# Optimization experiments

Hardware: AMD Instinct MI355X
Metric: run time of the kernel (lower is better)

The kernel has to match this reference:

```python
import jax, jax.numpy as jnp
import numpy as np

B, T, D, SD, CHUNK = 4, 4096, 1024, 512, 32


def setup_inputs() -> dict:
    key = jax.random.key(0)
    ks = jax.random.split(key, 6)
    sc_in = 1.0 / np.sqrt(D)
    sc_out = 1.0 / np.sqrt(2 * SD)
    return {
        "x": jax.random.normal(ks[0], (B, T, D), jnp.float32),
        "Wt": jax.random.normal(ks[1], (D, SD), jnp.float32) * sc_in,
        "bt": jnp.zeros((SD,), jnp.float32),
        "Wr": jax.random.normal(ks[2], (D, SD), jnp.float32) * sc_in,
        "br": jnp.zeros((SD,), jnp.float32),
        "Wi": jax.random.normal(ks[3], (D, 2 * SD), jnp.float32) * sc_in,
        "bi": jnp.zeros((2 * SD,), jnp.float32),
        "Wo": jax.random.normal(ks[4], (2 * SD, D), jnp.float32) * sc_out,
        "bo": jnp.zeros((D,), jnp.float32),
        "gamma": jnp.ones((D,), jnp.float32),
        "beta": jnp.zeros((D,), jnp.float32),
    }


def _rotation_scan(theta, retain, b_r, b_i, chunk):
    # theta/retain/b_*: [B, T, d]. Chunked linear recurrence h[t]=a[t]*h[t-1]+b[t]
    # with a[t] = retain[t]*e^{i theta[t]}, done in log-magnitude/angle space.
    Bsz, Tlen, d = theta.shape
    K = min(chunk, Tlen)
    n = Tlen // K  # T assumed divisible by K (4096 / 32)
    resh = lambda a: a.reshape(Bsz, n, K, d).transpose(1, 0, 2, 3)  # [n,B,K,d]
    th_c, rt_c, br_c, bi_c = resh(theta), resh(retain), resh(b_r), resh(b_i)

    def step(carry, xs):
        h_r, h_i = carry  # [B, d]
        th, rt, cb_r, cb_i = xs  # [B, K, d]
        cum_log_mag = jnp.cumsum(jnp.log(jnp.clip(rt, 1e-6, None)), axis=1)
        cum_mag = jnp.exp(cum_log_mag)
        cum_th = jnp.cumsum(th, axis=1)
        cum_cos = jnp.cos(cum_th)
        cum_sin = jnp.sin(cum_th)
        cum_a_r = cum_mag * cum_cos
        cum_a_i = cum_mag * cum_sin
        inv_mag = 1.0 / jnp.clip(cum_mag, 1e-8, None)
        inv_r = inv_mag * cum_cos          # cos(-t) = cos(t)
        inv_i = -inv_mag * cum_sin         # sin(-t) = -sin(t)
        scaled_b_r = inv_r * cb_r - inv_i * cb_i
        scaled_b_i = inv_r * cb_i + inv_i * cb_r
        cum_b_r = jnp.cumsum(scaled_b_r, axis=1)
        cum_b_i = jnp.cumsum(scaled_b_i, axis=1)
        tot_r = h_r[:, None] + cum_b_r
        tot_i = h_i[:, None] + cum_b_i
        ch_r = cum_a_r * tot_r - cum_a_i * tot_i
        ch_i = cum_a_r * tot_i + cum_a_i * tot_r
        return (ch_r[:, -1], ch_i[:, -1]), (ch_r, ch_i)

    h0 = (jnp.zeros((Bsz, d), theta.dtype), jnp.zeros((Bsz, d), theta.dtype))
    _, (out_r, out_i) = jax.lax.scan(step, h0, (th_c, rt_c, br_c, bi_c))
    back = lambda a: a.transpose(1, 0, 2, 3).reshape(Bsz, Tlen, d)
    return back(out_r), back(out_i)


def reference(x, Wt, bt, Wr, br, Wi, bi, Wo, bo, gamma, beta):
    d = Wt.shape[1]
    theta = x @ Wt + bt                       # [B,T,d]
    retain = jax.nn.sigmoid(x @ Wr + br)      # [B,T,d]
    inp = x @ Wi + bi                          # [B,T,2d]
    inp_r, inp_i = inp[..., :d], inp[..., d:]
    drive = 1.0 - retain
    out_r, out_i = _rotation_scan(theta, retain, drive * inp_r, drive * inp_i, CHUNK)
    out = jnp.concatenate([out_r, out_i], axis=-1)  # [B,T,2d]
    y = x + out @ Wo + bo
    mu = jnp.mean(y, axis=-1, keepdims=True)
    var = jnp.var(y, axis=-1, keepdims=True)
    return (y - mu) / jnp.sqrt(var + 1e-5) * gamma + beta
```

## Files before the change

kernel.cpp:

```cpp
#include <hip/hip_runtime.h>
#include <cstdint>


typedef __bf16 bf16x8 __attribute__((ext_vector_type(8)));
typedef float  f32x4  __attribute__((ext_vector_type(4)));
typedef ushort u16x8  __attribute__((ext_vector_type(8)));

#define AS1 __attribute__((address_space(1)))
#define AS3 __attribute__((address_space(3)))

__device__ __forceinline__ void gload16(const void* g, void* l) {
  __builtin_amdgcn_global_load_lds((const AS1 void*)g, (AS3 void*)l, 16, 0, 0);
}

__device__ __forceinline__ ushort f2bf(float f) {
  union { float f; uint32_t u; } v; v.f = f;
  uint32_t u = v.u;
  uint32_t r = u + 0x7FFFu + ((u >> 16) & 1u);
  return (ushort)(r >> 16);
}
__device__ __forceinline__ float bf2f(ushort u) {
  union { uint32_t x; float f; } v; v.x = (uint32_t)u << 16; return v.f;
}

__global__ __launch_bounds__(256) void tconv(const float* __restrict__ src, int R, int C,
                                             ushort* __restrict__ dst, int row_off) {
  __shared__ float tile[32][33];
  int tx = threadIdx.x, ty = threadIdx.y;
  int rb = blockIdx.y * 32, cb = blockIdx.x * 32;
#pragma unroll
  for (int yy = 0; yy < 4; ++yy) {
    int r = rb + ty + yy * 8;
    tile[ty + yy * 8][tx] = src[(size_t)r * C + cb + tx];
  }
  __syncthreads();
#pragma unroll
  for (int yy = 0; yy < 4; ++yy) {
    int c = cb + ty + yy * 8;
    dst[(size_t)(row_off + c) * R + rb + tx] = f2bf(tile[tx][ty + yy * 8]);
  }
}

__global__ __launch_bounds__(256) void pack_bias(const float* __restrict__ bt,
                                                 const float* __restrict__ br,
                                                 const float* __restrict__ bi,
                                                 float* __restrict__ bcat) {
  int i = blockIdx.x * 256 + threadIdx.x;
  bcat[i] = (i < 512) ? bt[i] : (i < 1024 ? br[i - 512] : bi[i - 1024]);
}

__global__ __launch_bounds__(256) void xconv(const float4* __restrict__ src,
                                             ushort* __restrict__ dst, int n4) {
  int i = blockIdx.x * 256 + threadIdx.x;
  if (i < n4) {
    float4 v = src[i];
    ushort4 o;
    o.x = f2bf(v.x); o.y = f2bf(v.y); o.z = f2bf(v.z); o.w = f2bf(v.w);
    *(ushort4*)(dst + (size_t)i * 4) = o;
  }
}

template <int BM>
__global__ __launch_bounds__(512, 2) void gemm256(const ushort* __restrict__ A,
                                                  const ushort* __restrict__ Bt,
                                                  ushort* __restrict__ C,
                                                  const float* __restrict__ bias,
                                                  int M, int N, int K, int nbn) {
  constexpr int MI = BM / 32;
  constexpr int II = BM / 128;
  constexpr int STAGE_USH = 2 * (BM * 64 + 256 * 64);
  constexpr int CT_USH = BM * 256;
  constexpr int SM_USH = (STAGE_USH > CT_USH) ? STAGE_USH : CT_USH;
  __shared__ alignas(16) ushort smem[SM_USH];
  ushort* const As0 = smem;
  ushort* const Bs0 = smem + 2 * BM * 64;

  const int cpx = gridDim.x >> 3;
  const int wg = ((int)blockIdx.x & 7) * cpx + ((int)blockIdx.x >> 3);
  const int bm = wg / nbn, bn = wg % nbn;

  const int t = threadIdx.x;
  const int l = t & 63, w = t >> 6;
  const int wm = w >> 2, wn = w & 3;
  const int r = l & 15, kq = l >> 4;

  const size_t a0 = (size_t)bm * BM * K;
  const size_t b0 = (size_t)bn * 256 * K;

  const int srow = t >> 3;
  const int sslot = (t & 7) ^ (srow & 7);
  const ushort* gA = A + a0 + (size_t)srow * K + sslot * 8;
  const ushort* gB = Bt + b0 + (size_t)srow * K + sslot * 8;
  const int lboff = w * 1024 + l * 16;

  f32x4 acc[MI][4] = {};
  const int NKT = K >> 6;

#define STGA(buf, kt, u) \
  gload16(gA + (size_t)((u) * 64) * K + (size_t)(kt) * 64, \
          (char*)(As0 + (buf) * BM * 64) + (u) * 8192 + lboff)
#define STGB(buf, kt, u) \
  gload16(gB + (size_t)((u) * 64) * K + (size_t)(kt) * 64, \
          (char*)(Bs0 + (buf) * 256 * 64) + (u) * 8192 + lboff)

#define QUAD(ph)                                                               \
  do {                                                                         \
    _Pragma("unroll")                                                          \
    for (int ii = 0; ii < II; ++ii) {                                          \
      bf16x8 aF[2];                                                            \
      const int rowa = wm * (BM / 2) + ((ph) * II + ii) * 16 + r;              \
      _Pragma("unroll")                                                        \
      for (int ks = 0; ks < 2; ++ks) {                                         \
        const int j = (ks * 4 + kq) ^ (r & 7);                                 \
        aF[ks] = *(const bf16x8*)&pA[rowa * 64 + j * 8];                       \
      }                                                                        \
      __builtin_amdgcn_s_setprio(1);                                           \
      _Pragma("unroll")                                                        \
      for (int jn = 0; jn < 4; ++jn)                                           \
        _Pragma("unroll")                                                      \
        for (int ks = 0; ks < 2; ++ks)                                         \
          acc[(ph) * II + ii][jn] = __builtin_amdgcn_mfma_f32_16x16x32_bf16(   \
              aF[ks], bF[jn][ks], acc[(ph) * II + ii][jn], 0, 0, 0);           \
      __builtin_amdgcn_s_setprio(0);                                           \
    }                                                                          \
  } while (0)

  STGB(0, 0, 0); STGB(0, 0, 1); STGB(0, 0, 2); STGB(0, 0, 3);
  if constexpr (BM == 256) { STGA(0, 0, 0); STGA(0, 0, 2); STGA(0, 0, 1); STGA(0, 0, 3); }
  else                     { STGA(0, 0, 0); STGA(0, 0, 1); }

  for (int kt = 0; kt < NKT; ++kt) {
    const int cur = kt & 1, nxt = cur ^ 1;
    const bool hn = (kt + 1 < NKT);
    const ushort* pA = As0 + cur * BM * 64;
    const ushort* pB = Bs0 + cur * 256 * 64;
    if (hn) { STGB(nxt, kt + 1, 0); STGB(nxt, kt + 1, 1); }
    if constexpr (BM == 256) {
      if (hn) asm volatile("s_waitcnt vmcnt(4)" ::: "memory");
      else    asm volatile("s_waitcnt vmcnt(2)" ::: "memory");
    } else {
      if (hn) asm volatile("s_waitcnt vmcnt(2)" ::: "memory");
      else    asm volatile("s_waitcnt vmcnt(0)" ::: "memory");
    }
    __builtin_amdgcn_s_barrier();
    asm volatile("" ::: "memory");
    bf16x8 bF[4][2];
#pragma unroll
    for (int jn = 0; jn < 4; ++jn) {
      const int rowb = wn * 64 + jn * 16 + r;
#pragma unroll
      for (int ks = 0; ks < 2; ++ks) {
        const int j = (ks * 4 + kq) ^ (r & 7);
        bF[jn][ks] = *(const bf16x8*)&pB[rowb * 64 + j * 8];
      }
    }
    QUAD(0);
    if (hn) { STGB(nxt, kt + 1, 2); STGB(nxt, kt + 1, 3); }
    QUAD(1);
    if (hn) {
      if constexpr (BM == 256) { STGA(nxt, kt + 1, 0); STGA(nxt, kt + 1, 2); }
      else                     { STGA(nxt, kt + 1, 0); }
    }
    if constexpr (BM == 256) {
      if (hn) asm volatile("s_waitcnt vmcnt(6)" ::: "memory");
      else    asm volatile("s_waitcnt vmcnt(0)" ::: "memory");
    }
    __builtin_amdgcn_s_barrier();
    asm volatile("" ::: "memory");
    QUAD(2);
    if (hn) {
      if constexpr (BM == 256) { STGA(nxt, kt + 1, 1); STGA(nxt, kt + 1, 3); }
      else                     { STGA(nxt, kt + 1, 1); }
    }
    QUAD(3);
  }
#undef STGA
#undef STGB
#undef QUAD

  asm volatile("s_waitcnt lgkmcnt(0) vmcnt(0)" ::: "memory");
  __builtin_amdgcn_s_barrier();

  const int q4 = (l >> 4) * 4;
  float bvj[4];
#pragma unroll
  for (int jn = 0; jn < 4; ++jn) {
    const int col = wn * 64 + jn * 16 + r;
    bvj[jn] = bias ? bias[bn * 256 + col] : 0.f;
  }
#pragma unroll
  for (int i = 0; i < MI; ++i) {
#pragma unroll
    for (int jn = 0; jn < 4; ++jn) {
      const int col = wn * 64 + jn * 16 + r;
      const int chunk = col >> 3;
#pragma unroll
      for (int q = 0; q < 4; ++q) {
        const int rowl = wm * (BM / 2) + i * 16 + q4 + q;
        const int pch = chunk ^ (rowl & 7);
        smem[rowl * 256 + pch * 8 + (col & 7)] = f2bf(acc[i][jn][q] + bvj[jn]);
      }
    }
  }
  __builtin_amdgcn_s_barrier();

  const int rrow0 = t >> 5;
  const int rch = t & 31;
#pragma unroll
  for (int p = 0; p < BM / 16; ++p) {
    const int rowl = p * 16 + rrow0;
    const int pch = rch ^ (rowl & 7);
    u16x8 vv = *(const u16x8*)&smem[rowl * 256 + pch * 8];
    const size_t grow = (size_t)(bm * BM + rowl);
    *(u16x8*)&C[grow * N + bn * 256 + rch * 8] = vv;
  }
}

__global__ __launch_bounds__(256) void scan_k1(const ushort* __restrict__ lin,
                                               float4* __restrict__ agg) {
  int bd = blockIdx.x * 256 + threadIdx.x;
  int c  = blockIdx.y;
  int b  = bd >> 9, d = bd & 511;
  const ushort* base = lin + ((size_t)b * 4096 + (size_t)c * 32) * 2048;
  float cth = 0.f, cbr = 0.f, cbi = 0.f;
  float cm = 1.f, cs = 1.f, sn = 0.f;
#pragma unroll 4
  for (int t = 0; t < 32; ++t) {
    const ushort* row = base + (size_t)t * 2048;
    float th = bf2f(row[d]);
    float z  = bf2f(row[512 + d]);
    float ir = bf2f(row[1024 + d]);
    float ii = bf2f(row[1536 + d]);
    float rt = __fdividef(1.f, 1.f + __expf(-z));
    cm *= fmaxf(rt, 1e-6f);
    cth += th;
    float s_, c_;
    __sincosf(cth, &s_, &c_);
    float im = __fdividef(1.f, fmaxf(cm, 1e-8f));
    float invr = im * c_, invi = -im * s_;
    float drive = 1.f - rt;
    float br_ = drive * ir, bi_ = drive * ii;
    cbr += invr * br_ - invi * bi_;
    cbi += invr * bi_ + invi * br_;
    cs = c_; sn = s_;
  }
  agg[(size_t)c * 2048 + bd] = make_float4(cm * cs, cm * sn, cbr, cbi);
}

__global__ __launch_bounds__(256) void scan_k2(const float4* __restrict__ agg,
                                               float2* __restrict__ h0) {
  int bd = blockIdx.x * 256 + threadIdx.x;
  float hr = 0.f, hi = 0.f;
  for (int cg = 0; cg < 16; ++cg) {
    float4 a[8];
#pragma unroll
    for (int u = 0; u < 8; ++u) a[u] = agg[(size_t)(cg * 8 + u) * 2048 + bd];
#pragma unroll
    for (int u = 0; u < 8; ++u) {
      h0[(size_t)(cg * 8 + u) * 2048 + bd] = make_float2(hr, hi);
      float tr = hr + a[u].z, ti = hi + a[u].w;
      hr = a[u].x * tr - a[u].y * ti;
      hi = a[u].x * ti + a[u].y * tr;
    }
  }
}

__global__ __launch_bounds__(256) void scan_k3(const ushort* __restrict__ lin,
                                               const float2* __restrict__ h0,
                                               ushort* __restrict__ outb) {
  int bd = blockIdx.x * 256 + threadIdx.x;
  int c  = blockIdx.y;
  int b  = bd >> 9, d = bd & 511;
  const ushort* base = lin + ((size_t)b * 4096 + (size_t)c * 32) * 2048;
  float2 h = h0[(size_t)c * 2048 + bd];
  float cth = 0.f, cbr = 0.f, cbi = 0.f, cm = 1.f;
#pragma unroll 4
  for (int t = 0; t < 32; ++t) {
    const ushort* row = base + (size_t)t * 2048;
    float th = bf2f(row[d]);
    float z  = bf2f(row[512 + d]);
    float ir = bf2f(row[1024 + d]);
    float ii = bf2f(row[1536 + d]);
    float rt = __fdividef(1.f, 1.f + __expf(-z));
    cm *= fmaxf(rt, 1e-6f);
    cth += th;
    float s_, c_;
    __sincosf(cth, &s_, &c_);
    float im = __fdividef(1.f, fmaxf(cm, 1e-8f));
    float invr = im * c_, invi = -im * s_;
    float drive = 1.f - rt;
    float br_ = drive * ir, bi_ = drive * ii;
    cbr += invr * br_ - invi * bi_;
    cbi += invr * bi_ + invi * br_;
    float ar = cm * c_, ai = cm * s_;
    float tr = h.x + cbr, ti = h.y + cbi;
    float orr = ar * tr - ai * ti;
    float oii = ar * ti + ai * tr;
    size_t rowo = ((size_t)b * 4096 + (size_t)c * 32 + t) * 1024;
    outb[rowo + d] = f2bf(orr);
    outb[rowo + 512 + d] = f2bf(oii);
  }
}

__global__ __launch_bounds__(256) void ln_k(const ushort* __restrict__ yb,
                                            const ushort* __restrict__ xb,
                                            const float* __restrict__ gamma,
                                            const float* __restrict__ beta,
                                            float* __restrict__ out) {
  int row = blockIdx.x;
  ushort4 uy = ((const ushort4*)(yb + (size_t)row * 1024))[threadIdx.x];
  ushort4 ux = ((const ushort4*)(xb + (size_t)row * 1024))[threadIdx.x];
  float4 v;
  v.x = bf2f(uy.x) + bf2f(ux.x);
  v.y = bf2f(uy.y) + bf2f(ux.y);
  v.z = bf2f(uy.z) + bf2f(ux.z);
  v.w = bf2f(uy.w) + bf2f(ux.w);
  float s  = v.x + v.y + v.z + v.w;
  float s2 = v.x * v.x + v.y * v.y + v.z * v.z + v.w * v.w;
#pragma unroll
  for (int off = 32; off > 0; off >>= 1) {
    s  += __shfl_down(s, off);
    s2 += __shfl_down(s2, off);
  }
  __shared__ float red[8];
  __shared__ float mv[2];
  int l = threadIdx.x & 63, w = threadIdx.x >> 6;
  if (l == 0) { red[w] = s; red[4 + w] = s2; }
  __syncthreads();
  if (threadIdx.x == 0) {
    float ts = red[0] + red[1] + red[2] + red[3];
    float t2 = red[4] + red[5] + red[6] + red[7];
    float mu = ts * (1.f / 1024.f);
    float var = t2 * (1.f / 1024.f) - mu * mu;
    mv[0] = mu;
    mv[1] = 1.f / sqrtf(var + 1e-5f);
  }
  __syncthreads();
  float mu = mv[0], rstd = mv[1];
  const float4* g4 = (const float4*)gamma;
  const float4* b4 = (const float4*)beta;
  float4 gv = g4[threadIdx.x], bv = b4[threadIdx.x];
  float4 o;
  o.x = (v.x - mu) * rstd * gv.x + bv.x;
  o.y = (v.y - mu) * rstd * gv.y + bv.y;
  o.z = (v.z - mu) * rstd * gv.z + bv.z;
  o.w = (v.w - mu) * rstd * gv.w + bv.w;
  ((float4*)(out + (size_t)row * 1024))[threadIdx.x] = o;
}

extern "C" void kernel_launch(void* const* d_in, const int* in_sizes, int n_in,
                              void* d_out, int out_size, void* d_ws, size_t ws_size,
                              hipStream_t stream) {
  (void)in_sizes; (void)n_in; (void)out_size; (void)ws_size;
  const float* x  = (const float*)d_in[0];
  const float* Wt = (const float*)d_in[1];
  const float* bt = (const float*)d_in[2];
  const float* Wr = (const float*)d_in[3];
  const float* br = (const float*)d_in[4];
  const float* Wi = (const float*)d_in[5];
  const float* bi = (const float*)d_in[6];
  const float* Wo = (const float*)d_in[7];
  const float* bo = (const float*)d_in[8];
  const float* gamma = (const float*)d_in[9];
  const float* beta  = (const float*)d_in[10];

  char* ws = (char*)d_ws;
  ushort* wcat_t = (ushort*)(ws);
  ushort* wo_t   = (ushort*)(ws + ((size_t)4  << 20));
  float*  bcat   = (float*) (ws + ((size_t)6  << 20));
  float4* agg    = (float4*)(ws + ((size_t)8  << 20));
  float2* h0     = (float2*)(ws + ((size_t)12 << 20));
  ushort* xb     = (ushort*)(ws + ((size_t)16 << 20));
  ushort* outb   = (ushort*)(ws + ((size_t)48 << 20));
  ushort* linb   = (ushort*)(ws + ((size_t)80 << 20));
  ushort* yb     = (ushort*)(ws + ((size_t)80 << 20));

  tconv<<<dim3(512 / 32, 1024 / 32), dim3(32, 8), 0, stream>>>(Wt, 1024, 512, wcat_t, 0);
  tconv<<<dim3(512 / 32, 1024 / 32), dim3(32, 8), 0, stream>>>(Wr, 1024, 512, wcat_t, 512);
  tconv<<<dim3(1024 / 32, 1024 / 32), dim3(32, 8), 0, stream>>>(Wi, 1024, 1024, wcat_t, 1024);
  tconv<<<dim3(1024 / 32, 1024 / 32), dim3(32, 8), 0, stream>>>(Wo, 1024, 1024, wo_t, 0);
  pack_bias<<<8, 256, 0, stream>>>(bt, br, bi, bcat);
  xconv<<<16384, 256, 0, stream>>>((const float4*)x, xb, 4194304);

  gemm256<256><<<512, 512, 0, stream>>>(xb, wcat_t, linb, bcat, 16384, 2048, 1024, 8);

  scan_k1<<<dim3(8, 128), 256, 0, stream>>>(linb, agg);
  scan_k2<<<8, 256, 0, stream>>>(agg, h0);
  scan_k3<<<dim3(8, 128), 256, 0, stream>>>(linb, h0, outb);

  gemm256<256><<<256, 512, 0, stream>>>(outb, wo_t, yb, bo, 16384, 1024, 1024, 4);

  ln_k<<<16384, 256, 0, stream>>>(yb, xb, gamma, beta, (float*)d_out);
}
```

Measured before the change: 210.6 us.

## Merge weight-transpose launches, reorder GEMM A-stage loads, use warp-per-row layernorm

The four weight transpose/convert launches become one 3D-grid kernel. In the GEMM main loop, the A fragments for the third quarter are read into registers before the next-stage A loads are issued, which drops one vmcnt wait and keeps MFMAs running across the barrier. The layernorm now gives each wavefront a full row and reduces with xor shuffles, removing shared-memory reductions and both __syncthreads. Together these aim to cut launch overhead and sync stalls, at the cost of a more fragile hand-written load/wait ordering in the GEMM.

```diff
diff --git a/kernel.cpp b/kernel.cpp
--- a/kernel.cpp
+++ b/kernel.cpp
@@ -23,8 +23,19 @@
   union { uint32_t x; float f; } v; v.x = (uint32_t)u << 16; return v.f;
 }
 
-__global__ __launch_bounds__(256) void tconv(const float* __restrict__ src, int R, int C,
-                                             ushort* __restrict__ dst, int row_off) {
+__global__ __launch_bounds__(256) void tconv_all(const float* __restrict__ Wt,
+                                                 const float* __restrict__ Wr,
+                                                 const float* __restrict__ Wi,
+                                                 const float* __restrict__ Wo,
+                                                 ushort* __restrict__ wcat,
+                                                 ushort* __restrict__ wot) {
+  const int z = blockIdx.z;
+  if (z < 2 && blockIdx.x >= 16) return;
+  const float* src = (z == 0) ? Wt : (z == 1) ? Wr : (z == 2) ? Wi : Wo;
+  const int C = (z < 2) ? 512 : 1024;
+  const int row_off = (z == 0) ? 0 : (z == 1) ? 512 : (z == 2) ? 1024 : 0;
+  ushort* dst = (z == 3) ? wot : wcat;
+
   __shared__ float tile[32][33];
   int tx = threadIdx.x, ty = threadIdx.y;
   int rb = blockIdx.y * 32, cb = blockIdx.x * 32;
@@ -37,7 +48,7 @@
 #pragma unroll
   for (int yy = 0; yy < 4; ++yy) {
     int c = cb + ty + yy * 8;
-    dst[(size_t)(row_off + c) * R + rb + tx] = f2bf(tile[tx][ty + yy * 8]);
+    dst[(size_t)(row_off + c) * 1024 + rb + tx] = f2bf(tile[tx][ty + yy * 8]);
   }
 }
 
@@ -60,20 +71,14 @@
   }
 }
 
-template <int BM>
 __global__ __launch_bounds__(512, 2) void gemm256(const ushort* __restrict__ A,
                                                   const ushort* __restrict__ Bt,
                                                   ushort* __restrict__ C,
                                                   const float* __restrict__ bias,
                                                   int M, int N, int K, int nbn) {
-  constexpr int MI = BM / 32;
-  constexpr int II = BM / 128;
-  constexpr int STAGE_USH = 2 * (BM * 64 + 256 * 64);
-  constexpr int CT_USH = BM * 256;
-  constexpr int SM_USH = (STAGE_USH > CT_USH) ? STAGE_USH : CT_USH;
-  __shared__ alignas(16) ushort smem[SM_USH];
+  __shared__ alignas(16) ushort smem[65536];
   ushort* const As0 = smem;
-  ushort* const Bs0 = smem + 2 * BM * 64;
+  ushort* const Bs0 = smem + 2 * 256 * 64;
 
   const int cpx = gridDim.x >> 3;
   const int wg = ((int)blockIdx.x & 7) * cpx + ((int)blockIdx.x >> 3);
@@ -84,7 +89,7 @@
   const int wm = w >> 2, wn = w & 3;
   const int r = l & 15, kq = l >> 4;
 
-  const size_t a0 = (size_t)bm * BM * K;
+  const size_t a0 = (size_t)bm * 256 * K;
   const size_t b0 = (size_t)bn * 256 * K;
 
   const int srow = t >> 3;
@@ -93,12 +98,12 @@
   const ushort* gB = Bt + b0 + (size_t)srow * K + sslot * 8;
   const int lboff = w * 1024 + l * 16;
 
-  f32x4 acc[MI][4] = {};
+  f32x4 acc[8][4] = {};
   const int NKT = K >> 6;
 
 #define STGA(buf, kt, u) \
   gload16(gA + (size_t)((u) * 64) * K + (size_t)(kt) * 64, \
-          (char*)(As0 + (buf) * BM * 64) + (u) * 8192 + lboff)
+          (char*)(As0 + (buf) * 256 * 64) + (u) * 8192 + lboff)
 #define STGB(buf, kt, u) \
   gload16(gB + (size_t)((u) * 64) * K + (size_t)(kt) * 64, \
           (char*)(Bs0 + (buf) * 256 * 64) + (u) * 8192 + lboff)
@@ -106,9 +111,9 @@
 #define QUAD(ph)                                                               \
   do {                                                                         \
     _Pragma("unroll")                                                          \
-    for (int ii = 0; ii < II; ++ii) {                                          \
+    for (int ii = 0; ii < 2; ++ii) {                                           \
       bf16x8 aF[2];                                                            \
-      const int rowa = wm * (BM / 2) + ((ph) * II + ii) * 16 + r;              \
+      const int rowa = wm * 128 + ((ph) * 2 + ii) * 16 + r;                    \
       _Pragma("unroll")                                                        \
       for (int ks = 0; ks < 2; ++ks) {                                         \
         const int j = (ks * 4 + kq) ^ (r & 7);                                 \
@@ -119,29 +124,24 @@
       for (int jn = 0; jn < 4; ++jn)                                           \
         _Pragma("unroll")                                                      \
         for (int ks = 0; ks < 2; ++ks)                                         \
-          acc[(ph) * II + ii][jn] = __builtin_amdgcn_mfma_f32_16x16x32_bf16(   \
-              aF[ks], bF[jn][ks], acc[(ph) * II + ii][jn], 0, 0, 0);           \
+          acc[(ph) * 2 + ii][jn] = __builtin_amdgcn_mfma_f32_16x16x32_bf16(    \
+              aF[ks], bF[jn][ks], acc[(ph) * 2 + ii][jn], 0, 0, 0);            \
       __builtin_amdgcn_s_setprio(0);                                           \
     }                                                                          \
   } while (0)
 
   STGB(0, 0, 0); STGB(0, 0, 1); STGB(0, 0, 2); STGB(0, 0, 3);
-  if constexpr (BM == 256) { STGA(0, 0, 0); STGA(0, 0, 2); STGA(0, 0, 1); STGA(0, 0, 3); }
-  else                     { STGA(0, 0, 0); STGA(0, 0, 1); }
+  STGA(0, 0, 0); STGA(0, 0, 2); STGA(0, 0, 1); STGA(0, 0, 3);
 
   for (int kt = 0; kt < NKT; ++kt) {
     const int cur = kt & 1, nxt = cur ^ 1;
     const bool hn = (kt + 1 < NKT);
-    const ushort* pA = As0 + cur * BM * 64;
+    const ushort* pA = As0 + cur * 256 * 64;
     const ushort* pB = Bs0 + cur * 256 * 64;
+
     if (hn) { STGB(nxt, kt + 1, 0); STGB(nxt, kt + 1, 1); }
-    if constexpr (BM == 256) {
-      if (hn) asm volatile("s_waitcnt vmcnt(4)" ::: "memory");
-      else    asm volatile("s_waitcnt vmcnt(2)" ::: "memory");
-    } else {
-      if (hn) asm volatile("s_waitcnt vmcnt(2)" ::: "memory");
-      else    asm volatile("s_waitcnt vmcnt(0)" ::: "memory");
-    }
+    if (hn) asm volatile("s_waitcnt vmcnt(2)" ::: "memory");
+    else    asm volatile("s_waitcnt vmcnt(0)" ::: "memory");
     __builtin_amdgcn_s_barrier();
     asm volatile("" ::: "memory");
     bf16x8 bF[4][2];
@@ -157,21 +157,30 @@
     QUAD(0);
     if (hn) { STGB(nxt, kt + 1, 2); STGB(nxt, kt + 1, 3); }
     QUAD(1);
-    if (hn) {
-      if constexpr (BM == 256) { STGA(nxt, kt + 1, 0); STGA(nxt, kt + 1, 2); }
-      else                     { STGA(nxt, kt + 1, 0); }
+    bf16x8 aFn[2][2];
+#pragma unroll
+    for (int ii = 0; ii < 2; ++ii) {
+      const int rowa = wm * 128 + (4 + ii) * 16 + r;
+#pragma unroll
+      for (int ks = 0; ks < 2; ++ks) {
+        const int j = (ks * 4 + kq) ^ (r & 7);
+        aFn[ii][ks] = *(const bf16x8*)&pA[rowa * 64 + j * 8];
+      }
     }
-    if constexpr (BM == 256) {
-      if (hn) asm volatile("s_waitcnt vmcnt(6)" ::: "memory");
-      else    asm volatile("s_waitcnt vmcnt(0)" ::: "memory");
-    }
+    if (hn) { STGA(nxt, kt + 1, 0); STGA(nxt, kt + 1, 2); }
+    asm volatile("" ::: "memory");
     __builtin_amdgcn_s_barrier();
-    asm volatile("" ::: "memory");
-    QUAD(2);
-    if (hn) {
-      if constexpr (BM == 256) { STGA(nxt, kt + 1, 1); STGA(nxt, kt + 1, 3); }
-      else                     { STGA(nxt, kt + 1, 1); }
-    }
+    __builtin_amdgcn_s_setprio(1);
+#pragma unroll
+    for (int ii = 0; ii < 2; ++ii)
+#pragma unroll
+      for (int jn = 0; jn < 4; ++jn)
+#pragma unroll
+        for (int ks = 0; ks < 2; ++ks)
+          acc[4 + ii][jn] = __builtin_amdgcn_mfma_f32_16x16x32_bf16(
+              aFn[ii][ks], bF[jn][ks], acc[4 + ii][jn], 0, 0, 0);
+    __builtin_amdgcn_s_setprio(0);
+    if (hn) { STGA(nxt, kt + 1, 1); STGA(nxt, kt + 1, 3); }
     QUAD(3);
   }
 #undef STGA
@@ -189,14 +198,14 @@
     bvj[jn] = bias ? bias[bn * 256 + col] : 0.f;
   }
 #pragma unroll
-  for (int i = 0; i < MI; ++i) {
+  for (int i = 0; i < 8; ++i) {
 #pragma unroll
     for (int jn = 0; jn < 4; ++jn) {
       const int col = wn * 64 + jn * 16 + r;
       const int chunk = col >> 3;
 #pragma unroll
       for (int q = 0; q < 4; ++q) {
-        const int rowl = wm * (BM / 2) + i * 16 + q4 + q;
+        const int rowl = wm * 128 + i * 16 + q4 + q;
         const int pch = chunk ^ (rowl & 7);
         smem[rowl * 256 + pch * 8 + (col & 7)] = f2bf(acc[i][jn][q] + bvj[jn]);
       }
@@ -207,11 +216,11 @@
   const int rrow0 = t >> 5;
   const int rch = t & 31;
 #pragma unroll
-  for (int p = 0; p < BM / 16; ++p) {
+  for (int p = 0; p < 16; ++p) {
     const int rowl = p * 16 + rrow0;
     const int pch = rch ^ (rowl & 7);
     u16x8 vv = *(const u16x8*)&smem[rowl * 256 + pch * 8];
-    const size_t grow = (size_t)(bm * BM + rowl);
+    const size_t grow = (size_t)(bm * 256 + rowl);
     *(u16x8*)&C[grow * N + bn * 256 + rch * 8] = vv;
   }
 }
@@ -307,45 +316,41 @@
                                             const float* __restrict__ gamma,
                                             const float* __restrict__ beta,
                                             float* __restrict__ out) {
-  int row = blockIdx.x;
-  ushort4 uy = ((const ushort4*)(yb + (size_t)row * 1024))[threadIdx.x];
-  ushort4 ux = ((const ushort4*)(xb + (size_t)row * 1024))[threadIdx.x];
-  float4 v;
-  v.x = bf2f(uy.x) + bf2f(ux.x);
-  v.y = bf2f(uy.y) + bf2f(ux.y);
-  v.z = bf2f(uy.z) + bf2f(ux.z);
-  v.w = bf2f(uy.w) + bf2f(ux.w);
-  float s  = v.x + v.y + v.z + v.w;
-  float s2 = v.x * v.x + v.y * v.y + v.z * v.z + v.w * v.w;
+  const int lane = threadIdx.x & 63;
+  const size_t row = (size_t)blockIdx.x * 4 + (threadIdx.x >> 6);
+  const ushort* yr = yb + row * 1024;
+  const ushort* xr = xb + row * 1024;
+  float v[4][4];
+  float s = 0.f, s2 = 0.f;
+#pragma unroll
+  for (int q = 0; q < 4; ++q) {
+    ushort4 uy = *(const ushort4*)(yr + q * 256 + lane * 4);
+    ushort4 ux = *(const ushort4*)(xr + q * 256 + lane * 4);
+    v[q][0] = bf2f(uy.x) + bf2f(ux.x);
+    v[q][1] = bf2f(uy.y) + bf2f(ux.y);
+    v[q][2] = bf2f(uy.z) + bf2f(ux.z);
+    v[q][3] = bf2f(uy.w) + bf2f(ux.w);
+#pragma unroll
+    for (int j = 0; j < 4; ++j) { s += v[q][j]; s2 += v[q][j] * v[q][j]; }
+  }
 #pragma unroll
   for (int off = 32; off > 0; off >>= 1) {
-    s  += __shfl_down(s, off);
-    s2 += __shfl_down(s2, off);
-  }
-  __shared__ float red[8];
-  __shared__ float mv[2];
-  int l = threadIdx.x & 63, w = threadIdx.x >> 6;
-  if (l == 0) { red[w] = s; red[4 + w] = s2; }
-  __syncthreads();
-  if (threadIdx.x == 0) {
-    float ts = red[0] + red[1] + red[2] + red[3];
-    float t2 = red[4] + red[5] + red[6] + red[7];
-    float mu = ts * (1.f / 1024.f);
-    float var = t2 * (1.f / 1024.f) - mu * mu;
-    mv[0] = mu;
-    mv[1] = 1.f / sqrtf(var + 1e-5f);
-  }
-  __syncthreads();
-  float mu = mv[0], rstd = mv[1];
-  const float4* g4 = (const float4*)gamma;
-  const float4* b4 = (const float4*)beta;
-  float4 gv = g4[threadIdx.x], bv = b4[threadIdx.x];
-  float4 o;
-  o.x = (v.x - mu) * rstd * gv.x + bv.x;
-  o.y = (v.y - mu) * rstd * gv.y + bv.y;
-  o.z = (v.z - mu) * rstd * gv.z + bv.z;
-  o.w = (v.w - mu) * rstd * gv.w + bv.w;
-  ((float4*)(out + (size_t)row * 1024))[threadIdx.x] = o;
+    s  += __shfl_xor(s, off);
+    s2 += __shfl_xor(s2, off);
+  }
+  const float mu = s * (1.f / 1024.f);
+  const float rstd = rsqrtf(s2 * (1.f / 1024.f) - mu * mu + 1e-5f);
+#pragma unroll
+  for (int q = 0; q < 4; ++q) {
+    float4 gv = *(const float4*)(gamma + q * 256 + lane * 4);
+    float4 bv = *(const float4*)(beta + q * 256 + lane * 4);
+    float4 o;
+    o.x = (v[q][0] - mu) * rstd * gv.x + bv.x;
+    o.y = (v[q][1] - mu) * rstd * gv.y + bv.y;
+    o.z = (v[q][2] - mu) * rstd * gv.z + bv.z;
+    o.w = (v[q][3] - mu) * rstd * gv.w + bv.w;
+    *(float4*)(out + row * 1024 + q * 256 + lane * 4) = o;
+  }
 }
 
 extern "C" void kernel_launch(void* const* d_in, const int* in_sizes, int n_in,
@@ -375,20 +380,17 @@
   ushort* linb   = (ushort*)(ws + ((size_t)80 << 20));
   ushort* yb     = (ushort*)(ws + ((size_t)80 << 20));
 
-  tconv<<<dim3(512 / 32, 1024 / 32), dim3(32, 8), 0, stream>>>(Wt, 1024, 512, wcat_t, 0);
-  tconv<<<dim3(512 / 32, 1024 / 32), dim3(32, 8), 0, stream>>>(Wr, 1024, 512, wcat_t, 512);
-  tconv<<<dim3(1024 / 32, 1024 / 32), dim3(32, 8), 0, stream>>>(Wi, 1024, 1024, wcat_t, 1024);
-  tconv<<<dim3(1024 / 32, 1024 / 32), dim3(32, 8), 0, stream>>>(Wo, 1024, 1024, wo_t, 0);
+  tconv_all<<<dim3(32, 32, 4), dim3(32, 8), 0, stream>>>(Wt, Wr, Wi, Wo, wcat_t, wo_t);
   pack_bias<<<8, 256, 0, stream>>>(bt, br, bi, bcat);
   xconv<<<16384, 256, 0, stream>>>((const float4*)x, xb, 4194304);
 
-  gemm256<256><<<512, 512, 0, stream>>>(xb, wcat_t, linb, bcat, 16384, 2048, 1024, 8);
+  gemm256<<<512, 512, 0, stream>>>(xb, wcat_t, linb, bcat, 16384, 2048, 1024, 8);
 
   scan_k1<<<dim3(8, 128), 256, 0, stream>>>(linb, agg);
   scan_k2<<<8, 256, 0, stream>>>(agg, h0);
   scan_k3<<<dim3(8, 128), 256, 0, stream>>>(linb, h0, outb);
 
-  gemm256<256><<<256, 512, 0, stream>>>(outb, wo_t, yb, bo, 16384, 1024, 1024, 4);
-
-  ln_k<<<16384, 256, 0, stream>>>(yb, xb, gamma, beta, (float*)d_out);
-}
+  gemm256<<<256, 512, 0, stream>>>(outb, wo_t, yb, bo, 16384, 1024, 1024, 4);
+
+  ln_k<<<4096, 256, 0, stream>>>(yb, xb, gamma, beta, (float*)d_out);
+}
```

After: 199.3 us. 5.3% less time.
